# Optimization experiments

Hardware: AMD Instinct MI355X
Metric: run time of the kernel (lower is better)

The kernel has to match this reference:

```python
import jax, jax.numpy as jnp
import numpy as np

B, C, H, W = 32, 64, 96, 96
RED = 8


def setup_inputs() -> dict:
    key = jax.random.key(0)
    k0, k1, k2 = jax.random.split(key, 3)
    x = jax.random.normal(k0, (B, C, H, W), dtype=jnp.float32)
    # 1x1 conv weights (squeezed to linear): conv1 C->C//RED, conv2 C//RED->C
    w1 = jax.random.normal(k1, (C // RED, C), dtype=jnp.float32) * (1.0 / np.sqrt(C))
    b1 = jnp.zeros((C // RED,), dtype=jnp.float32)
    w2 = jax.random.normal(k2, (C, C // RED), dtype=jnp.float32) * (1.0 / np.sqrt(C // RED))
    b2 = jnp.zeros((C,), dtype=jnp.float32)
    return {"x": x, "w1": w1, "b1": b1, "w2": w2, "b2": b2}


def reference(x, w1, b1, w2, b2):
    Bx, Cx, Hx, Wx = x.shape
    M = Hx * Wx
    # --- covariance pooling: x @ I_hat @ x^T == centered outer product / M ---
    xr = x.reshape(Bx, Cx, M)
    xc = xr - xr.mean(axis=-1, keepdims=True)
    cov = jnp.einsum('bcm,bdm->bcd', xc, xc) / M  # (B, C, C)
    # --- Newton-Schulz matrix sqrt, iteration = 5 ---
    I3 = 3.0 * jnp.eye(Cx, dtype=x.dtype)  # broadcast over batch
    normA = jnp.trace(cov, axis1=1, axis2=2)  # (1/3 * cov * 3I).sum == trace
    A = cov / normA[:, None, None]
    ZY = 0.5 * (I3 - A)
    Y = A @ ZY
    Z = ZY
    for _ in range(3):  # range(1, iteration-1) with iteration=5
        ZY = (0.5 * (I3 - Z)) @ Y
        Y = Y @ ZY
        Z = ZY @ Z
    ZY = 0.5 * (Y @ (I3 - Z @ Y))
    cov_sqrt = ZY * jnp.sqrt(normA)[:, None, None]  # (B, C, C)
    # --- channel gating ---
    s = cov_sqrt.mean(axis=1)  # mean over dim=1 -> (B, C)
    h = jax.nn.relu(s @ w1.T + b1)
    gate = jax.nn.sigmoid(h @ w2.T + b2)  # (B, C)
    return x * gate[:, :, None, None]
```

## Files before the change

### kernel.cpp

```cpp
#include <hip/hip_runtime.h>
#include <math.h>


#define BB 32
#define CC 64
#define MM 9216

typedef __attribute__((ext_vector_type(8))) short bf16x8;
typedef __attribute__((ext_vector_type(4))) float f32x4;

__device__ __forceinline__ short f2bf(float f) {
  unsigned u = __builtin_bit_cast(unsigned, f);
  return (short)(unsigned short)((u + 0x8000u) >> 16);
}
__device__ __forceinline__ float bf2f(short h) {
  unsigned u = ((unsigned)(unsigned short)h) << 16;
  return __builtin_bit_cast(float, u);
}

#define NCHUNKS 16

template <int NSTEP>
__device__ __forceinline__ void gram_body(const float* __restrict__ xb, int mwave,
                                          int quad, int col,
                                          f32x4 acc[4][4], float csum[4]) {
  const float* base[4];
#pragma unroll
  for (int rb = 0; rb < 4; rb++)
    base[rb] = xb + (size_t)(rb * 16 + col) * MM + mwave + quad * 8;

  float4 cur[4][2];
#pragma unroll
  for (int rb = 0; rb < 4; rb++) {
    cur[rb][0] = *(const float4*)(base[rb]);
    cur[rb][1] = *(const float4*)(base[rb] + 4);
  }
#pragma unroll
  for (int s = 0; s < NSTEP; s++) {
    float4 nxt[4][2];
    if (s + 1 < NSTEP) {
#pragma unroll
      for (int rb = 0; rb < 4; rb++) {
        const float* p = base[rb] + (s + 1) * 32;
        nxt[rb][0] = *(const float4*)(p);
        nxt[rb][1] = *(const float4*)(p + 4);
      }
    }
    bf16x8 frag[4];
#pragma unroll
    for (int rb = 0; rb < 4; rb++) {
      float v0 = cur[rb][0].x, v1 = cur[rb][0].y, v2 = cur[rb][0].z, v3 = cur[rb][0].w;
      float v4 = cur[rb][1].x, v5 = cur[rb][1].y, v6 = cur[rb][1].z, v7 = cur[rb][1].w;
      csum[rb] += ((v0 + v1) + (v2 + v3)) + ((v4 + v5) + (v6 + v7));
      bf16x8 f;
      f[0] = f2bf(v0); f[1] = f2bf(v1); f[2] = f2bf(v2); f[3] = f2bf(v3);
      f[4] = f2bf(v4); f[5] = f2bf(v5); f[6] = f2bf(v6); f[7] = f2bf(v7);
      frag[rb] = f;
    }
#pragma unroll
    for (int i = 0; i < 4; i++)
#pragma unroll
      for (int j = 0; j < 4; j++)
        acc[i][j] = __builtin_amdgcn_mfma_f32_16x16x32_bf16(frag[i], frag[j],
                                                            acc[i][j], 0, 0, 0);
    if (s + 1 < NSTEP) {
#pragma unroll
      for (int rb = 0; rb < 4; rb++) {
        cur[rb][0] = nxt[rb][0];
        cur[rb][1] = nxt[rb][1];
      }
    }
  }
}

__global__ __launch_bounds__(256, 2) void gram_k(const float* __restrict__ x,
                                                 float* __restrict__ covws,
                                                 float* __restrict__ sumws) {
  int b = blockIdx.x / NCHUNKS;
  int chunk = blockIdx.x % NCHUNKS;
  int tid = threadIdx.x;
  int w = tid >> 6, lane = tid & 63;
  int quad = lane >> 4, col = lane & 15;
  const float* xb = x + (size_t)b * CC * MM;

  f32x4 acc[4][4];
#pragma unroll
  for (int i = 0; i < 4; i++)
#pragma unroll
    for (int j = 0; j < 4; j++) acc[i][j] = (f32x4){0.f, 0.f, 0.f, 0.f};
  float csum[4] = {0.f, 0.f, 0.f, 0.f};

  if (chunk < 8) {
    int mwave = chunk * 640 + w * (5 * 32);
    gram_body<5>(xb, mwave, quad, col, acc, csum);
  } else {
    int mwave = 5120 + (chunk - 8) * 512 + w * (4 * 32);
    gram_body<4>(xb, mwave, quad, col, acc, csum);
  }

  __shared__ float red[4][4096];
#pragma unroll
  for (int i = 0; i < 4; i++)
#pragma unroll
    for (int j = 0; j < 4; j++)
#pragma unroll
      for (int r = 0; r < 4; r++)
        red[w][(i * 16 + quad * 4 + r) * 64 + j * 16 + col] = acc[i][j][r];
  __syncthreads();
  float* covb = covws + b * 4096;
#pragma unroll
  for (int e = 0; e < 16; e++) {
    int idx = tid + 256 * e;
    float v = (red[0][idx] + red[1][idx]) + (red[2][idx] + red[3][idx]);
    atomicAdd(covb + idx, v);
  }
#pragma unroll
  for (int rb = 0; rb < 4; rb++) {
    float c0 = csum[rb];
    c0 += __shfl_xor(c0, 16);
    c0 += __shfl_xor(c0, 32);
    if (quad == 0) {
      if (lane < 16) atomicAdd(sumws + b * 64 + rb * 16 + lane, c0);
    }
  }
}

__device__ __forceinline__ void mm64(short* __restrict__ D, const short* __restrict__ A,
                                     const short* __restrict__ Bm, int tid) {
  int w = tid >> 6, lane = tid & 63, quad = lane >> 4, col = lane & 15;
  f32x4 acc[4];
#pragma unroll
  for (int j = 0; j < 4; j++) acc[j] = (f32x4){0.f, 0.f, 0.f, 0.f};
#pragma unroll
  for (int ks = 0; ks < 2; ks++) {
    int k0 = ks * 32 + quad * 8;
    bf16x8 fa = *(const bf16x8*)(A + (w * 16 + col) * 64 + k0);
#pragma unroll
    for (int j = 0; j < 4; j++) {
      bf16x8 fb = *(const bf16x8*)(Bm + (j * 16 + col) * 64 + k0);
      acc[j] = __builtin_amdgcn_mfma_f32_16x16x32_bf16(fa, fb, acc[j], 0, 0, 0);
    }
  }
#pragma unroll
  for (int j = 0; j < 4; j++)
#pragma unroll
    for (int r = 0; r < 4; r++)
      D[(w * 16 + quad * 4 + r) * 64 + j * 16 + col] = f2bf(acc[j][r]);
}

__device__ __forceinline__ void mmcolsum(const short* __restrict__ A,
                                         const short* __restrict__ Bm,
                                         float* scol, int tid) {
  int w = tid >> 6, lane = tid & 63, quad = lane >> 4, col = lane & 15;
  f32x4 acc[4];
#pragma unroll
  for (int j = 0; j < 4; j++) acc[j] = (f32x4){0.f, 0.f, 0.f, 0.f};
#pragma unroll
  for (int ks = 0; ks < 2; ks++) {
    int k0 = ks * 32 + quad * 8;
    bf16x8 fa = *(const bf16x8*)(A + (w * 16 + col) * 64 + k0);
#pragma unroll
    for (int j = 0; j < 4; j++) {
      bf16x8 fb = *(const bf16x8*)(Bm + (j * 16 + col) * 64 + k0);
      acc[j] = __builtin_amdgcn_mfma_f32_16x16x32_bf16(fa, fb, acc[j], 0, 0, 0);
    }
  }
#pragma unroll
  for (int j = 0; j < 4; j++) {
    float t = (acc[j][0] + acc[j][1]) + (acc[j][2] + acc[j][3]);
    atomicAdd(&scol[j * 16 + col], t);
  }
}

__global__ __launch_bounds__(256) void ns_k(const float* __restrict__ covws,
                                            const float* __restrict__ sumws,
                                            const float* __restrict__ w1,
                                            const float* __restrict__ pb1,
                                            const float* __restrict__ w2,
                                            const float* __restrict__ pb2,
                                            float* __restrict__ gatews) {
  __shared__ __align__(16) short nb0[4096], nb1[4096], nb2[4096], nb3[4096], nb4[4096];
  __shared__ float mu[64];
  __shared__ float scol[64];
  __shared__ float hbuf[8];
  __shared__ float normA_sh;
  int b = blockIdx.x;
  int tid = threadIdx.x;
  const float* gram = covws + b * 4096;

  if (tid < 64) mu[tid] = sumws[b * 64 + tid] * (1.0f / MM);
  __syncthreads();
  if (tid < 64) {
    float d = gram[tid * 65] * (1.0f / MM) - mu[tid] * mu[tid];
#pragma unroll
    for (int off = 32; off >= 1; off >>= 1) d += __shfl_down(d, off);
    if (tid == 0) normA_sh = d;
  }
  __syncthreads();
  float rn = 1.0f / normA_sh;
#pragma unroll
  for (int e = 0; e < 16; e++) {
    int idx = tid + 256 * e;
    int r = idx >> 6, c = idx & 63;
    float cv = gram[idx] * (1.0f / MM) - mu[r] * mu[c];
    float a = cv * rn;
    nb0[idx] = f2bf(a);
    nb1[idx] = f2bf((r == c ? 1.5f : 0.0f) - 0.5f * a);
  }
  __syncthreads();
  mm64(nb2, nb0, nb1, tid);
  __syncthreads();
  short *pY = nb2, *pZ = nb1, *s0 = nb3, *s1 = nb4, *s2 = nb0;
  for (int it = 0; it < 3; ++it) {
#pragma unroll
    for (int e = 0; e < 16; e++) {
      int idx = tid + 256 * e;
      int r = idx >> 6, c = idx & 63;
      float z = bf2f(pZ[idx]);
      s0[idx] = f2bf((r == c ? 1.5f : 0.0f) - 0.5f * z);
    }
    __syncthreads();
    mm64(s1, s0, pY, tid);
    __syncthreads();
    mm64(s2, pY, s1, tid);
    mm64(s0, s1, pZ, tid);
    __syncthreads();
    short* oY = pY; short* oZ = pZ; short* oW = s1;
    pY = s2; pZ = s0; s0 = oY; s1 = oZ; s2 = oW;
  }
  mm64(s0, pZ, pY, tid);
  __syncthreads();
#pragma unroll
  for (int e = 0; e < 16; e++) {
    int idx = tid + 256 * e;
    int r = idx >> 6, c = idx & 63;
    float p = bf2f(s0[idx]);
    s0[idx] = f2bf((r == c ? 3.0f : 0.0f) - p);
  }
  if (tid < 64) scol[tid] = 0.0f;
  __syncthreads();
  mmcolsum(pY, s0, scol, tid);
  __syncthreads();
  if (tid < 8) {
    float sc = 0.5f * sqrtf(normA_sh) * (1.0f / 64.0f);
    float acc = pb1[tid];
    for (int c = 0; c < 64; c++) acc += scol[c] * sc * w1[tid * 64 + c];
    hbuf[tid] = fmaxf(acc, 0.0f);
  }
  __syncthreads();
  if (tid < 64) {
    float acc = pb2[tid];
#pragma unroll
    for (int j = 0; j < 8; j++) acc += hbuf[j] * w2[tid * 8 + j];
    gatews[b * 64 + tid] = 1.0f / (1.0f + __expf(-acc));
  }
}

#define N4 (BB * CC * MM / 4)
__global__ __launch_bounds__(256) void gate_mul(const float* __restrict__ x,
                                                const float* __restrict__ gatews,
                                                float* __restrict__ out) {
  int i = blockIdx.x * 256 + threadIdx.x;
  int bc = i / 2304;
  float g = gatews[bc];
  float4 v = ((const float4*)x)[i];
  v.x *= g; v.y *= g; v.z *= g; v.w *= g;
  ((float4*)out)[i] = v;
}

extern "C" void kernel_launch(void* const* d_in, const int* in_sizes, int n_in,
                              void* d_out, int out_size, void* d_ws, size_t ws_size,
                              hipStream_t stream) {
  const float* x = (const float*)d_in[0];
  const float* w1 = (const float*)d_in[1];
  const float* b1 = (const float*)d_in[2];
  const float* w2 = (const float*)d_in[3];
  const float* b2 = (const float*)d_in[4];
  float* out = (float*)d_out;
  float* ws = (float*)d_ws;
  float* covws = ws;
  float* sumws = ws + BB * 4096;
  float* gatews = sumws + BB * 64;

  hipMemsetAsync(ws, 0, (size_t)(BB * 4096 + BB * 64) * sizeof(float), stream);
  gram_k<<<BB * NCHUNKS, 256, 0, stream>>>(x, covws, sumws);
  ns_k<<<BB, 256, 0, stream>>>(covws, sumws, w1, b1, w2, b2, gatews);
  gate_mul<<<N4 / 256, 256, 0, stream>>>(x, gatews, out);
}
```

Before: 166.9 us.

## Fuse Newton-Schulz stage into gram kernel via last-block-done counter

Merges the covariance accumulation and the Newton-Schulz/gating computation into one kernel. A per-batch atomic counter lets the last of the 16 chunk blocks for each batch run the matrix-sqrt and gate computation, reusing the shared memory buffer. This removes one kernel launch and its serialization gap. The gate multiply kernel is also changed so each block handles one (b,c) plane with 9 float4 loads per thread, replacing the per-element division used to find the gate index. The trade-off is that the tail of the gram kernel now runs the serial NS work on only 32 blocks, and relaxed atomic loads are used to read the accumulated results.

Result: slower. 239.0 us (+43.2%).

```diff
diff --git a/kernel.cpp b/kernel.cpp
--- a/kernel.cpp
+++ b/kernel.cpp
@@ -16,6 +16,56 @@
 __device__ __forceinline__ float bf2f(short h) {
   unsigned u = ((unsigned)(unsigned short)h) << 16;
   return __builtin_bit_cast(float, u);
+}
+__device__ __forceinline__ float gload(const float* p) {
+  return __hip_atomic_load(p, __ATOMIC_RELAXED, __HIP_MEMORY_SCOPE_AGENT);
+}
+
+__device__ __forceinline__ void mm64(short* __restrict__ D, const short* __restrict__ A,
+                                     const short* __restrict__ Bm, int tid) {
+  int w = tid >> 6, lane = tid & 63, quad = lane >> 4, col = lane & 15;
+  f32x4 acc[4];
+#pragma unroll
+  for (int j = 0; j < 4; j++) acc[j] = (f32x4){0.f, 0.f, 0.f, 0.f};
+#pragma unroll
+  for (int ks = 0; ks < 2; ks++) {
+    int k0 = ks * 32 + quad * 8;
+    bf16x8 fa = *(const bf16x8*)(A + (w * 16 + col) * 64 + k0);
+#pragma unroll
+    for (int j = 0; j < 4; j++) {
+      bf16x8 fb = *(const bf16x8*)(Bm + (j * 16 + col) * 64 + k0);
+      acc[j] = __builtin_amdgcn_mfma_f32_16x16x32_bf16(fa, fb, acc[j], 0, 0, 0);
+    }
+  }
+#pragma unroll
+  for (int j = 0; j < 4; j++)
+#pragma unroll
+    for (int r = 0; r < 4; r++)
+      D[(w * 16 + quad * 4 + r) * 64 + j * 16 + col] = f2bf(acc[j][r]);
+}
+
+__device__ __forceinline__ void mmcolsum(const short* __restrict__ A,
+                                         const short* __restrict__ Bm,
+                                         float* scol, int tid) {
+  int w = tid >> 6, lane = tid & 63, quad = lane >> 4, col = lane & 15;
+  f32x4 acc[4];
+#pragma unroll
+  for (int j = 0; j < 4; j++) acc[j] = (f32x4){0.f, 0.f, 0.f, 0.f};
+#pragma unroll
+  for (int ks = 0; ks < 2; ks++) {
+    int k0 = ks * 32 + quad * 8;
+    bf16x8 fa = *(const bf16x8*)(A + (w * 16 + col) * 64 + k0);
+#pragma unroll
+    for (int j = 0; j < 4; j++) {
+      bf16x8 fb = *(const bf16x8*)(Bm + (j * 16 + col) * 64 + k0);
+      acc[j] = __builtin_amdgcn_mfma_f32_16x16x32_bf16(fa, fb, acc[j], 0, 0, 0);
+    }
+  }
+#pragma unroll
+  for (int j = 0; j < 4; j++) {
+    float t = (acc[j][0] + acc[j][1]) + (acc[j][2] + acc[j][3]);
+    atomicAdd(&scol[j * 16 + col], t);
+  }
 }
 
 #define NCHUNKS 16
@@ -73,9 +123,15 @@
   }
 }
 
-__global__ __launch_bounds__(256, 2) void gram_k(const float* __restrict__ x,
-                                                 float* __restrict__ covws,
-                                                 float* __restrict__ sumws) {
+__global__ __launch_bounds__(256, 2) void gram_ns_k(
+    const float* __restrict__ x, float* __restrict__ covws,
+    float* __restrict__ sumws, int* __restrict__ ctr,
+    const float* __restrict__ w1, const float* __restrict__ pb1,
+    const float* __restrict__ w2, const float* __restrict__ pb2,
+    float* __restrict__ gatews) {
+  __shared__ __align__(16) unsigned char smem[65536];
+  float(*red)[4096] = reinterpret_cast<float(*)[4096]>(smem);
+
   int b = blockIdx.x / NCHUNKS;
   int chunk = blockIdx.x % NCHUNKS;
   int tid = threadIdx.x;
@@ -98,7 +154,6 @@
     gram_body<4>(xb, mwave, quad, col, acc, csum);
   }
 
-  __shared__ float red[4][4096];
 #pragma unroll
   for (int i = 0; i < 4; i++)
 #pragma unroll
@@ -123,86 +178,43 @@
       if (lane < 16) atomicAdd(sumws + b * 64 + rb * 16 + lane, c0);
     }
   }
-}
-
-__device__ __forceinline__ void mm64(short* __restrict__ D, const short* __restrict__ A,
-                                     const short* __restrict__ Bm, int tid) {
-  int w = tid >> 6, lane = tid & 63, quad = lane >> 4, col = lane & 15;
-  f32x4 acc[4];
-#pragma unroll
-  for (int j = 0; j < 4; j++) acc[j] = (f32x4){0.f, 0.f, 0.f, 0.f};
-#pragma unroll
-  for (int ks = 0; ks < 2; ks++) {
-    int k0 = ks * 32 + quad * 8;
-    bf16x8 fa = *(const bf16x8*)(A + (w * 16 + col) * 64 + k0);
-#pragma unroll
-    for (int j = 0; j < 4; j++) {
-      bf16x8 fb = *(const bf16x8*)(Bm + (j * 16 + col) * 64 + k0);
-      acc[j] = __builtin_amdgcn_mfma_f32_16x16x32_bf16(fa, fb, acc[j], 0, 0, 0);
-    }
-  }
-#pragma unroll
-  for (int j = 0; j < 4; j++)
-#pragma unroll
-    for (int r = 0; r < 4; r++)
-      D[(w * 16 + quad * 4 + r) * 64 + j * 16 + col] = f2bf(acc[j][r]);
-}
-
-__device__ __forceinline__ void mmcolsum(const short* __restrict__ A,
-                                         const short* __restrict__ Bm,
-                                         float* scol, int tid) {
-  int w = tid >> 6, lane = tid & 63, quad = lane >> 4, col = lane & 15;
-  f32x4 acc[4];
-#pragma unroll
-  for (int j = 0; j < 4; j++) acc[j] = (f32x4){0.f, 0.f, 0.f, 0.f};
-#pragma unroll
-  for (int ks = 0; ks < 2; ks++) {
-    int k0 = ks * 32 + quad * 8;
-    bf16x8 fa = *(const bf16x8*)(A + (w * 16 + col) * 64 + k0);
-#pragma unroll
-    for (int j = 0; j < 4; j++) {
-      bf16x8 fb = *(const bf16x8*)(Bm + (j * 16 + col) * 64 + k0);
-      acc[j] = __builtin_amdgcn_mfma_f32_16x16x32_bf16(fa, fb, acc[j], 0, 0, 0);
-    }
-  }
-#pragma unroll
-  for (int j = 0; j < 4; j++) {
-    float t = (acc[j][0] + acc[j][1]) + (acc[j][2] + acc[j][3]);
-    atomicAdd(&scol[j * 16 + col], t);
-  }
-}
-
-__global__ __launch_bounds__(256) void ns_k(const float* __restrict__ covws,
-                                            const float* __restrict__ sumws,
-                                            const float* __restrict__ w1,
-                                            const float* __restrict__ pb1,
-                                            const float* __restrict__ w2,
-                                            const float* __restrict__ pb2,
-                                            float* __restrict__ gatews) {
-  __shared__ __align__(16) short nb0[4096], nb1[4096], nb2[4096], nb3[4096], nb4[4096];
-  __shared__ float mu[64];
-  __shared__ float scol[64];
-  __shared__ float hbuf[8];
-  __shared__ float normA_sh;
-  int b = blockIdx.x;
-  int tid = threadIdx.x;
+
+  __threadfence();
+  __syncthreads();
+  int* pold = (int*)(smem + 41600);
+  if (tid == 0)
+    *pold = __hip_atomic_fetch_add(ctr + b, 1, __ATOMIC_ACQ_REL,
+                                   __HIP_MEMORY_SCOPE_AGENT);
+  __syncthreads();
+  if (*pold != NCHUNKS - 1) return;
+
+  short* nb0 = (short*)smem;
+  short* nb1 = nb0 + 4096;
+  short* nb2 = nb0 + 8192;
+  short* nb3 = nb0 + 12288;
+  short* nb4 = nb0 + 16384;
+  float* mu = (float*)(smem + 40960);
+  float* scol = (float*)(smem + 41216);
+  float* hbuf = (float*)(smem + 41472);
+  float* pnormA = (float*)(smem + 41504);
   const float* gram = covws + b * 4096;
 
-  if (tid < 64) mu[tid] = sumws[b * 64 + tid] * (1.0f / MM);
+  if (tid < 64) mu[tid] = gload(sumws + b * 64 + tid) * (1.0f / MM);
   __syncthreads();
   if (tid < 64) {
-    float d = gram[tid * 65] * (1.0f / MM) - mu[tid] * mu[tid];
+    float d = gload(gram + tid * 65) * (1.0f / MM) - mu[tid] * mu[tid];
 #pragma unroll
     for (int off = 32; off >= 1; off >>= 1) d += __shfl_down(d, off);
-    if (tid == 0) normA_sh = d;
-  }
-  __syncthreads();
-  float rn = 1.0f / normA_sh;
+    if (tid == 0) *pnormA = d;
+  }
+  __syncthreads();
+  float normA = *pnormA;
+  float rn = 1.0f / normA;
 #pragma unroll
   for (int e = 0; e < 16; e++) {
     int idx = tid + 256 * e;
     int r = idx >> 6, c = idx & 63;
-    float cv = gram[idx] * (1.0f / MM) - mu[r] * mu[c];
+    float cv = gload(gram + idx) * (1.0f / MM) - mu[r] * mu[c];
     float a = cv * rn;
     nb0[idx] = f2bf(a);
     nb1[idx] = f2bf((r == c ? 1.5f : 0.0f) - 0.5f * a);
@@ -242,30 +254,34 @@
   mmcolsum(pY, s0, scol, tid);
   __syncthreads();
   if (tid < 8) {
-    float sc = 0.5f * sqrtf(normA_sh) * (1.0f / 64.0f);
-    float acc = pb1[tid];
-    for (int c = 0; c < 64; c++) acc += scol[c] * sc * w1[tid * 64 + c];
-    hbuf[tid] = fmaxf(acc, 0.0f);
+    float sc = 0.5f * sqrtf(normA) * (1.0f / 64.0f);
+    float acc2 = pb1[tid];
+    for (int c = 0; c < 64; c++) acc2 += scol[c] * sc * w1[tid * 64 + c];
+    hbuf[tid] = fmaxf(acc2, 0.0f);
   }
   __syncthreads();
   if (tid < 64) {
-    float acc = pb2[tid];
-#pragma unroll
-    for (int j = 0; j < 8; j++) acc += hbuf[j] * w2[tid * 8 + j];
-    gatews[b * 64 + tid] = 1.0f / (1.0f + __expf(-acc));
-  }
-}
-
-#define N4 (BB * CC * MM / 4)
+    float acc2 = pb2[tid];
+#pragma unroll
+    for (int j = 0; j < 8; j++) acc2 += hbuf[j] * w2[tid * 8 + j];
+    gatews[b * 64 + tid] = 1.0f / (1.0f + __expf(-acc2));
+  }
+}
+
 __global__ __launch_bounds__(256) void gate_mul(const float* __restrict__ x,
                                                 const float* __restrict__ gatews,
                                                 float* __restrict__ out) {
-  int i = blockIdx.x * 256 + threadIdx.x;
-  int bc = i / 2304;
+  int bc = blockIdx.x;
   float g = gatews[bc];
-  float4 v = ((const float4*)x)[i];
-  v.x *= g; v.y *= g; v.z *= g; v.w *= g;
-  ((float4*)out)[i] = v;
+  const float4* xp = (const float4*)(x + (size_t)bc * MM);
+  float4* op = (float4*)(out + (size_t)bc * MM);
+  int t = threadIdx.x;
+#pragma unroll
+  for (int it = 0; it < 9; ++it) {
+    float4 v = xp[t + it * 256];
+    v.x *= g; v.y *= g; v.z *= g; v.w *= g;
+    op[t + it * 256] = v;
+  }
 }
 
 extern "C" void kernel_launch(void* const* d_in, const int* in_sizes, int n_in,
@@ -280,10 +296,11 @@
   float* ws = (float*)d_ws;
   float* covws = ws;
   float* sumws = ws + BB * 4096;
-  float* gatews = sumws + BB * 64;
-
-  hipMemsetAsync(ws, 0, (size_t)(BB * 4096 + BB * 64) * sizeof(float), stream);
-  gram_k<<<BB * NCHUNKS, 256, 0, stream>>>(x, covws, sumws);
-  ns_k<<<BB, 256, 0, stream>>>(covws, sumws, w1, b1, w2, b2, gatews);
-  gate_mul<<<N4 / 256, 256, 0, stream>>>(x, gatews, out);
-}
+  int* ctr = (int*)(sumws + BB * 64);
+  float* gatews = (float*)(ctr + BB);
+
+  hipMemsetAsync(ws, 0, (size_t)(BB * 4096 + BB * 64 + BB) * sizeof(float), stream);
+  gram_ns_k<<<BB * NCHUNKS, 256, 0, stream>>>(x, covws, sumws, ctr, w1, b1, w2,
+                                              b2, gatews);
+  gate_mul<<<BB * CC, 256, 0, stream>>>(x, gatews, out);
+}
```

## Replace atomic cross-chunk reduction with per-chunk partials summed in NS kernel

Applied to the files above, without the earlier changes.

When the workspace is large enough, gram_k writes each chunk's partial Gram matrix and column sums to separate slots with plain stores. ns_k then sums the 16 partials per batch into shared memory, which removes the memset and the global float atomics. The partial reduction moves onto only 32 blocks that each read 16x16KB, which may serialise part of the cost. gate_mul is also restructured so that each block handles one (b,c) plane, giving it a single gate load and removing the integer division.

Result: no change. 168.7 us (+1.1%).

```diff
diff --git a/kernel.cpp b/kernel.cpp
--- a/kernel.cpp
+++ b/kernel.cpp
@@ -5,6 +5,7 @@
 #define BB 32
 #define CC 64
 #define MM 9216
+#define NCHUNKS 16
 
 typedef __attribute__((ext_vector_type(8))) short bf16x8;
 typedef __attribute__((ext_vector_type(4))) float f32x4;
@@ -17,8 +18,6 @@
   unsigned u = ((unsigned)(unsigned short)h) << 16;
   return __builtin_bit_cast(float, u);
 }
-
-#define NCHUNKS 16
 
 template <int NSTEP>
 __device__ __forceinline__ void gram_body(const float* __restrict__ xb, int mwave,
@@ -73,9 +72,10 @@
   }
 }
 
+template <bool PART>
 __global__ __launch_bounds__(256, 2) void gram_k(const float* __restrict__ x,
-                                                 float* __restrict__ covws,
-                                                 float* __restrict__ sumws) {
+                                                 float* __restrict__ pg,
+                                                 float* __restrict__ ps) {
   int b = blockIdx.x / NCHUNKS;
   int chunk = blockIdx.x % NCHUNKS;
   int tid = threadIdx.x;
@@ -99,6 +99,7 @@
   }
 
   __shared__ float red[4][4096];
+  __shared__ float cred[4][64];
 #pragma unroll
   for (int i = 0; i < 4; i++)
 #pragma unroll
@@ -106,21 +107,36 @@
 #pragma unroll
       for (int r = 0; r < 4; r++)
         red[w][(i * 16 + quad * 4 + r) * 64 + j * 16 + col] = acc[i][j][r];
-  __syncthreads();
-  float* covb = covws + b * 4096;
-#pragma unroll
-  for (int e = 0; e < 16; e++) {
-    int idx = tid + 256 * e;
-    float v = (red[0][idx] + red[1][idx]) + (red[2][idx] + red[3][idx]);
-    atomicAdd(covb + idx, v);
-  }
 #pragma unroll
   for (int rb = 0; rb < 4; rb++) {
     float c0 = csum[rb];
     c0 += __shfl_xor(c0, 16);
     c0 += __shfl_xor(c0, 32);
-    if (quad == 0) {
-      if (lane < 16) atomicAdd(sumws + b * 64 + rb * 16 + lane, c0);
+    if (lane < 16) cred[w][rb * 16 + lane] = c0;
+  }
+  __syncthreads();
+
+  if (PART) {
+    float* covb = pg + (size_t)blockIdx.x * 4096;
+#pragma unroll
+    for (int e = 0; e < 16; e++) {
+      int idx = tid + 256 * e;
+      covb[idx] = (red[0][idx] + red[1][idx]) + (red[2][idx] + red[3][idx]);
+    }
+    if (tid < 64)
+      ps[blockIdx.x * 64 + tid] =
+          (cred[0][tid] + cred[1][tid]) + (cred[2][tid] + cred[3][tid]);
+  } else {
+    float* covb = pg + (size_t)b * 4096;
+#pragma unroll
+    for (int e = 0; e < 16; e++) {
+      int idx = tid + 256 * e;
+      float v = (red[0][idx] + red[1][idx]) + (red[2][idx] + red[3][idx]);
+      atomicAdd(covb + idx, v);
+    }
+    if (tid < 64) {
+      float v = (cred[0][tid] + cred[1][tid]) + (cred[2][tid] + cred[3][tid]);
+      atomicAdd(ps + b * 64 + tid, v);
     }
   }
 }
@@ -172,37 +188,65 @@
   }
 }
 
-__global__ __launch_bounds__(256) void ns_k(const float* __restrict__ covws,
-                                            const float* __restrict__ sumws,
+template <bool PART>
+__global__ __launch_bounds__(256) void ns_k(const float* __restrict__ pg,
+                                            const float* __restrict__ ps,
                                             const float* __restrict__ w1,
                                             const float* __restrict__ pb1,
                                             const float* __restrict__ w2,
                                             const float* __restrict__ pb2,
                                             float* __restrict__ gatews) {
   __shared__ __align__(16) short nb0[4096], nb1[4096], nb2[4096], nb3[4096], nb4[4096];
+  __shared__ float gsum[4096];
   __shared__ float mu[64];
   __shared__ float scol[64];
   __shared__ float hbuf[8];
   __shared__ float normA_sh;
   int b = blockIdx.x;
   int tid = threadIdx.x;
-  const float* gram = covws + b * 4096;
-
-  if (tid < 64) mu[tid] = sumws[b * 64 + tid] * (1.0f / MM);
-  __syncthreads();
+
+  if (PART) {
+    const float* pgb = pg + (size_t)b * NCHUNKS * 4096;
+#pragma unroll
+    for (int e = 0; e < 16; e++) {
+      int idx = tid + 256 * e;
+      float s = 0.f;
+#pragma unroll
+      for (int c = 0; c < NCHUNKS; c++) s += pgb[c * 4096 + idx];
+      gsum[idx] = s;
+    }
+    if (tid < 64) {
+      const float* psb = ps + (size_t)b * NCHUNKS * 64;
+      float s = 0.f;
+#pragma unroll
+      for (int c = 0; c < NCHUNKS; c++) s += psb[c * 64 + tid];
+      mu[tid] = s * (1.0f / MM);
+    }
+  } else {
+    const float* gram = pg + (size_t)b * 4096;
+#pragma unroll
+    for (int e = 0; e < 16; e++) {
+      int idx = tid + 256 * e;
+      gsum[idx] = gram[idx];
+    }
+    if (tid < 64) mu[tid] = ps[b * 64 + tid] * (1.0f / MM);
+  }
+  __syncthreads();
+
   if (tid < 64) {
-    float d = gram[tid * 65] * (1.0f / MM) - mu[tid] * mu[tid];
+    float d = gsum[tid * 65] * (1.0f / MM) - mu[tid] * mu[tid];
 #pragma unroll
     for (int off = 32; off >= 1; off >>= 1) d += __shfl_down(d, off);
     if (tid == 0) normA_sh = d;
   }
   __syncthreads();
-  float rn = 1.0f / normA_sh;
+  float normA = normA_sh;
+  float rn = 1.0f / normA;
 #pragma unroll
   for (int e = 0; e < 16; e++) {
     int idx = tid + 256 * e;
     int r = idx >> 6, c = idx & 63;
-    float cv = gram[idx] * (1.0f / MM) - mu[r] * mu[c];
+    float cv = gsum[idx] * (1.0f / MM) - mu[r] * mu[c];
     float a = cv * rn;
     nb0[idx] = f2bf(a);
     nb1[idx] = f2bf((r == c ? 1.5f : 0.0f) - 0.5f * a);
@@ -242,30 +286,34 @@
   mmcolsum(pY, s0, scol, tid);
   __syncthreads();
   if (tid < 8) {
-    float sc = 0.5f * sqrtf(normA_sh) * (1.0f / 64.0f);
-    float acc = pb1[tid];
-    for (int c = 0; c < 64; c++) acc += scol[c] * sc * w1[tid * 64 + c];
-    hbuf[tid] = fmaxf(acc, 0.0f);
+    float sc = 0.5f * sqrtf(normA) * (1.0f / 64.0f);
+    float acc2 = pb1[tid];
+    for (int c = 0; c < 64; c++) acc2 += scol[c] * sc * w1[tid * 64 + c];
+    hbuf[tid] = fmaxf(acc2, 0.0f);
   }
   __syncthreads();
   if (tid < 64) {
-    float acc = pb2[tid];
-#pragma unroll
-    for (int j = 0; j < 8; j++) acc += hbuf[j] * w2[tid * 8 + j];
-    gatews[b * 64 + tid] = 1.0f / (1.0f + __expf(-acc));
-  }
-}
-
-#define N4 (BB * CC * MM / 4)
+    float acc2 = pb2[tid];
+#pragma unroll
+    for (int j = 0; j < 8; j++) acc2 += hbuf[j] * w2[tid * 8 + j];
+    gatews[b * 64 + tid] = 1.0f / (1.0f + __expf(-acc2));
+  }
+}
+
 __global__ __launch_bounds__(256) void gate_mul(const float* __restrict__ x,
                                                 const float* __restrict__ gatews,
                                                 float* __restrict__ out) {
-  int i = blockIdx.x * 256 + threadIdx.x;
-  int bc = i / 2304;
+  int bc = blockIdx.x;
   float g = gatews[bc];
-  float4 v = ((const float4*)x)[i];
-  v.x *= g; v.y *= g; v.z *= g; v.w *= g;
-  ((float4*)out)[i] = v;
+  const float4* xp = (const float4*)(x + (size_t)bc * MM);
+  float4* op = (float4*)(out + (size_t)bc * MM);
+  int t = threadIdx.x;
+#pragma unroll
+  for (int it = 0; it < 9; ++it) {
+    float4 v = xp[t + it * 256];
+    v.x *= g; v.y *= g; v.z *= g; v.w *= g;
+    op[t + it * 256] = v;
+  }
 }
 
 extern "C" void kernel_launch(void* const* d_in, const int* in_sizes, int n_in,
@@ -278,12 +326,25 @@
   const float* b2 = (const float*)d_in[4];
   float* out = (float*)d_out;
   float* ws = (float*)d_ws;
-  float* covws = ws;
-  float* sumws = ws + BB * 4096;
-  float* gatews = sumws + BB * 64;
-
-  hipMemsetAsync(ws, 0, (size_t)(BB * 4096 + BB * 64) * sizeof(float), stream);
-  gram_k<<<BB * NCHUNKS, 256, 0, stream>>>(x, covws, sumws);
-  ns_k<<<BB, 256, 0, stream>>>(covws, sumws, w1, b1, w2, b2, gatews);
-  gate_mul<<<N4 / 256, 256, 0, stream>>>(x, gatews, out);
-}
+
+  const size_t NPG = (size_t)BB * NCHUNKS * 4096;
+  const size_t NPS = (size_t)BB * NCHUNKS * 64;
+  const size_t needP = (NPG + NPS + BB * CC) * sizeof(float);
+
+  if (ws_size >= needP) {
+    float* pg = ws;
+    float* psum = ws + NPG;
+    float* gatews = psum + NPS;
+    gram_k<true><<<BB * NCHUNKS, 256, 0, stream>>>(x, pg, psum);
+    ns_k<true><<<BB, 256, 0, stream>>>(pg, psum, w1, b1, w2, b2, gatews);
+    gate_mul<<<BB * CC, 256, 0, stream>>>(x, gatews, out);
+  } else {
+    float* covws = ws;
+    float* sumws = ws + BB * 4096;
+    float* gatews = sumws + BB * 64;
+    hipMemsetAsync(ws, 0, (size_t)(BB * 4096 + BB * 64) * sizeof(float), stream);
+    gram_k<false><<<BB * NCHUNKS, 256, 0, stream>>>(x, covws, sumws);
+    ns_k<false><<<BB, 256, 0, stream>>>(covws, sumws, w1, b1, w2, b2, gatews);
+    gate_mul<<<BB * CC, 256, 0, stream>>>(x, gatews, out);
+  }
+}
```
